# Optimization experiments

Measured on AMD Instinct MI355X. Metric: run time of the kernel, lower is better.

## Reference

```python
import jax, jax.numpy as jnp
import numpy as np

EMBED_DIM = 1024
HIDDEN = 128
N_QUERY = 65536
N_PROTO = 512


def setup_inputs() -> dict:
    key = jax.random.key(0)
    k1, k2, k3, k4, k5, k6, k7 = jax.random.split(key, 7)
    d2 = EMBED_DIM * 2
    lim1 = 1.0 / np.sqrt(d2)
    lim2 = 1.0 / np.sqrt(HIDDEN)
    return {
        "query_features": jax.random.normal(k1, (N_QUERY, EMBED_DIM), dtype=jnp.float32),
        "prototypes": jax.random.normal(k2, (N_PROTO, EMBED_DIM), dtype=jnp.float32),
        "distances": jax.random.uniform(k3, (N_QUERY, N_PROTO), dtype=jnp.float32),
        "W1": jax.random.uniform(k4, (d2, HIDDEN), minval=-lim1, maxval=lim1, dtype=jnp.float32),
        "b1": jax.random.uniform(k5, (HIDDEN,), minval=-lim1, maxval=lim1, dtype=jnp.float32),
        "W2": jax.random.uniform(k6, (HIDDEN, 1), minval=-lim2, maxval=lim2, dtype=jnp.float32),
        "b2": jax.random.uniform(k7, (1,), minval=-lim2, maxval=lim2, dtype=jnp.float32),
    }


def reference(query_features, prototypes, distances, W1, b1, W2, b2):
    # Batched version of the per-query loop: argmin -> gather -> concat -> MLP.
    idx = jnp.argmin(distances, axis=1)                      # [N_QUERY]
    closest = prototypes[idx]                                # [N_QUERY, D]
    combined = jnp.concatenate([query_features, closest], axis=-1)  # [N_QUERY, 2D]
    h = jax.nn.relu(combined @ W1 + b1)                      # [N_QUERY, 128]
    out = jax.nn.sigmoid(h @ W2 + b2)                        # [N_QUERY, 1]
    return jnp.squeeze(out, axis=-1)                         # [N_QUERY]
```

## Files before the change

### kernel.cpp

```cpp
#include <hip/hip_runtime.h>
#include <hip/hip_bf16.h>
#include <math.h>

#define EMBED 1024
#define HIDDEN 128
#define NPROTO 512

typedef short bf16x8 __attribute__((ext_vector_type(8)));
typedef short bf16x4 __attribute__((ext_vector_type(4)));
typedef float f32x4 __attribute__((ext_vector_type(4)));

__device__ __forceinline__ unsigned short f2bf(float x) {
    unsigned u = __builtin_bit_cast(unsigned, x);
    unsigned r = u + 0x7FFFu + ((u >> 16) & 1u);
    return (unsigned short)(r >> 16);
}

__global__ __launch_bounds__(128) void prep_kernel(
    const float* __restrict__ prototypes,
    const float* __restrict__ W1,
    float* __restrict__ proto_h,
    unsigned short* __restrict__ w1t)
{
    int blk = blockIdx.x;
    int t = threadIdx.x;
    if (blk < 64) {
        __shared__ float pl[8][1024];
        int p0 = blk * 8;
        const float4* src = (const float4*)(prototypes + (size_t)p0 * EMBED);
        float4* dst = (float4*)(&pl[0][0]);
        #pragma unroll
        for (int i = 0; i < 16; ++i) dst[t + i * 128] = src[t + i * 128];
        __syncthreads();
        float acc[8] = {0.f,0.f,0.f,0.f,0.f,0.f,0.f,0.f};
        for (int k = 0; k < 1024; k += 8) {
            float w[8];
            #pragma unroll
            for (int j = 0; j < 8; ++j) w[j] = W1[(size_t)(1024 + k + j) * 128 + t];
            #pragma unroll
            for (int j = 0; j < 8; ++j) {
                #pragma unroll
                for (int p = 0; p < 8; ++p) acc[p] += pl[p][k + j] * w[j];
            }
        }
        #pragma unroll
        for (int p = 0; p < 8; ++p) proto_h[(size_t)(p0 + p) * 128 + t] = acc[p];
    } else {
        int b = blk - 64;
        #pragma unroll
        for (int i = 0; i < 16; ++i) {
            int flat = b * 2048 + i * 128 + t;
            int k = flat >> 7;
            int n = flat & 127;
            w1t[(size_t)n * 1024 + k] = f2bf(W1[(size_t)k * 128 + n]);
        }
    }
}

__global__ __launch_bounds__(256) void main_kernel(
    const float* __restrict__ qf,
    const float* __restrict__ dist,
    const float* __restrict__ b1,
    const float* __restrict__ W2,
    const float* __restrict__ b2,
    const float* __restrict__ proto_h,
    const unsigned short* __restrict__ w1t,
    float* __restrict__ out)
{
    const int LDA = 72;
    __shared__ unsigned short a_lds[128 * 72];
    __shared__ unsigned short b_lds[128 * 72];
    __shared__ int s_idx[128];
    __shared__ float s_red[128][2];

    int t = threadIdx.x;
    int wave = t >> 6, lane = t & 63;
    int blk = blockIdx.x;
    int q0 = blk * 128;

    for (int i = 0; i < 32; ++i) {
        int q = wave * 32 + i;
        const float* dr = dist + (size_t)(q0 + q) * 512;
        float4 v0 = ((const float4*)dr)[lane];
        float4 v1 = ((const float4*)dr)[lane + 64];
        float bv = v0.x; int bi = lane * 4;
        if (v0.y < bv) { bv = v0.y; bi = lane * 4 + 1; }
        if (v0.z < bv) { bv = v0.z; bi = lane * 4 + 2; }
        if (v0.w < bv) { bv = v0.w; bi = lane * 4 + 3; }
        int b1i = 256 + lane * 4;
        if (v1.x < bv) { bv = v1.x; bi = b1i; }
        if (v1.y < bv) { bv = v1.y; bi = b1i + 1; }
        if (v1.z < bv) { bv = v1.z; bi = b1i + 2; }
        if (v1.w < bv) { bv = v1.w; bi = b1i + 3; }
        #pragma unroll
        for (int s = 1; s < 64; s <<= 1) {
            float ov = __shfl_xor(bv, s);
            int   oi = __shfl_xor(bi, s);
            if (ov < bv || (ov == bv && oi < bi)) { bv = ov; bi = oi; }
        }
        if (lane == 0) s_idx[q] = bi;
    }

    int wave_m = wave >> 1, wave_n = wave & 1;
    int quad = lane >> 4, tid16 = lane & 15;
    f32x4 acc[4][4];
    #pragma unroll
    for (int mi = 0; mi < 4; ++mi)
        #pragma unroll
        for (int ni = 0; ni < 4; ++ni)
            acc[mi][ni] = (f32x4){0.f, 0.f, 0.f, 0.f};

    for (int kt = 0; kt < 1024; kt += 64) {
        #pragma unroll
        for (int i = 0; i < 8; ++i) {
            int m = (t >> 4) + i * 16;
            int k = (t & 15) * 4;
            float4 v = *(const float4*)(qf + (size_t)(q0 + m) * 1024 + kt + k);
            bf16x4 pk;
            pk.x = (short)f2bf(v.x); pk.y = (short)f2bf(v.y);
            pk.z = (short)f2bf(v.z); pk.w = (short)f2bf(v.w);
            *(bf16x4*)(&a_lds[m * LDA + k]) = pk;
        }
        #pragma unroll
        for (int i = 0; i < 4; ++i) {
            int n = (t >> 3) + i * 32;
            int k = (t & 7) * 8;
            bf16x8 v = *(const bf16x8*)(w1t + (size_t)n * 1024 + kt + k);
            *(bf16x8*)(&b_lds[n * LDA + k]) = v;
        }
        __syncthreads();

        #pragma unroll
        for (int ks = 0; ks < 2; ++ks) {
            int kk = ks * 32 + quad * 8;
            bf16x8 af[4], bfr[4];
            #pragma unroll
            for (int mi = 0; mi < 4; ++mi)
                af[mi] = *(bf16x8*)(&a_lds[(wave_m * 64 + mi * 16 + tid16) * LDA + kk]);
            #pragma unroll
            for (int ni = 0; ni < 4; ++ni)
                bfr[ni] = *(bf16x8*)(&b_lds[(wave_n * 64 + ni * 16 + tid16) * LDA + kk]);
            #pragma unroll
            for (int mi = 0; mi < 4; ++mi)
                #pragma unroll
                for (int ni = 0; ni < 4; ++ni)
                    acc[mi][ni] = __builtin_amdgcn_mfma_f32_16x16x32_bf16(
                        af[mi], bfr[ni], acc[mi][ni], 0, 0, 0);
        }
        __syncthreads();
    }

    float b1v[4], w2v[4];
    #pragma unroll
    for (int ni = 0; ni < 4; ++ni) {
        int n = wave_n * 64 + ni * 16 + tid16;
        b1v[ni] = b1[n];
        w2v[ni] = W2[n];
    }
    #pragma unroll
    for (int mi = 0; mi < 4; ++mi) {
        #pragma unroll
        for (int r = 0; r < 4; ++r) {
            int m = wave_m * 64 + mi * 16 + quad * 4 + r;
            const float* ph = proto_h + (size_t)s_idx[m] * 128;
            float sum = 0.f;
            #pragma unroll
            for (int ni = 0; ni < 4; ++ni) {
                int n = wave_n * 64 + ni * 16 + tid16;
                float v = acc[mi][ni][r] + b1v[ni] + ph[n];
                sum += fmaxf(v, 0.f) * w2v[ni];
            }
            #pragma unroll
            for (int s = 1; s < 16; s <<= 1) sum += __shfl_xor(sum, s);
            if (tid16 == 0) s_red[m][wave_n] = sum;
        }
    }
    __syncthreads();
    if (t < 128) {
        float s = s_red[t][0] + s_red[t][1] + b2[0];
        out[q0 + t] = 1.f / (1.f + expf(-s));
    }
}

extern "C" void kernel_launch(void* const* d_in, const int* in_sizes, int n_in,
                              void* d_out, int out_size, void* d_ws, size_t ws_size,
                              hipStream_t stream) {
    const float* qf    = (const float*)d_in[0];
    const float* proto = (const float*)d_in[1];
    const float* dist  = (const float*)d_in[2];
    const float* W1    = (const float*)d_in[3];
    const float* b1    = (const float*)d_in[4];
    const float* W2    = (const float*)d_in[5];
    const float* b2    = (const float*)d_in[6];
    float* out = (float*)d_out;

    float* proto_h = (float*)d_ws;
    unsigned short* w1t = (unsigned short*)((char*)d_ws + 512 * 128 * 4);

    prep_kernel<<<128, 128, 0, stream>>>(proto, W1, proto_h, w1t);

    int nq = in_sizes[0] / EMBED;
    main_kernel<<<nq / 128, 256, 0, stream>>>(qf, dist, b1, W2, b2, proto_h, w1t, out);
}
```

Measured before the change: 525.3 us.

## Double-buffer query tiles in LDS, load W1 fragments directly, batch argmin loads

The main kernel now double-buffers the bf16 query tile in LDS, prefetching the next K-slice of fp32 query features into registers while the MFMAs on the current slice run. There is one barrier per iteration instead of two. The B operand (transposed bf16 W1) is read straight from global/L2 into registers, so the B LDS tile goes away. The argmin over distances issues four rows' loads at once to raise memory-level parallelism, and the first query tile load is issued before the argmin. The prep kernel is also reorganized with more blocks and vectorized bf16x8 stores. Launch bounds now request 3 blocks per CU, which risks register pressure from the prefetch buffers.

```diff
diff --git a/kernel.cpp b/kernel.cpp
--- a/kernel.cpp
+++ b/kernel.cpp
@@ -5,9 +5,9 @@
 #define EMBED 1024
 #define HIDDEN 128
 #define NPROTO 512
+#define LDA 72
 
 typedef short bf16x8 __attribute__((ext_vector_type(8)));
-typedef short bf16x4 __attribute__((ext_vector_type(4)));
 typedef float f32x4 __attribute__((ext_vector_type(4)));
 
 __device__ __forceinline__ unsigned short f2bf(float x) {
@@ -16,48 +16,39 @@
     return (unsigned short)(r >> 16);
 }
 
-__global__ __launch_bounds__(128) void prep_kernel(
+__global__ __launch_bounds__(256) void prep_kernel(
     const float* __restrict__ prototypes,
     const float* __restrict__ W1,
     float* __restrict__ proto_h,
     unsigned short* __restrict__ w1t)
 {
-    int blk = blockIdx.x;
+    int b = blockIdx.x;
     int t = threadIdx.x;
-    if (blk < 64) {
-        __shared__ float pl[8][1024];
-        int p0 = blk * 8;
-        const float4* src = (const float4*)(prototypes + (size_t)p0 * EMBED);
-        float4* dst = (float4*)(&pl[0][0]);
-        #pragma unroll
-        for (int i = 0; i < 16; ++i) dst[t + i * 128] = src[t + i * 128];
-        __syncthreads();
-        float acc[8] = {0.f,0.f,0.f,0.f,0.f,0.f,0.f,0.f};
-        for (int k = 0; k < 1024; k += 8) {
-            float w[8];
-            #pragma unroll
-            for (int j = 0; j < 8; ++j) w[j] = W1[(size_t)(1024 + k + j) * 128 + t];
-            #pragma unroll
-            for (int j = 0; j < 8; ++j) {
-                #pragma unroll
-                for (int p = 0; p < 8; ++p) acc[p] += pl[p][k + j] * w[j];
-            }
-        }
-        #pragma unroll
-        for (int p = 0; p < 8; ++p) proto_h[(size_t)(p0 + p) * 128 + t] = acc[p];
+    if (b < 256) {
+        int ph = t >> 7, h = t & 127;
+        int p = b * 2 + ph;
+        const float* pr = prototypes + (size_t)p * EMBED;
+        const float* w  = W1 + (size_t)EMBED * HIDDEN + h;
+        float acc = 0.f;
+        for (int k = 0; k < EMBED; k += 8) {
+            #pragma unroll
+            for (int j = 0; j < 8; ++j)
+                acc += pr[k + j] * w[(size_t)(k + j) * HIDDEN];
+        }
+        proto_h[(size_t)p * HIDDEN + h] = acc;
     } else {
-        int b = blk - 64;
-        #pragma unroll
-        for (int i = 0; i < 16; ++i) {
-            int flat = b * 2048 + i * 128 + t;
-            int k = flat >> 7;
-            int n = flat & 127;
-            w1t[(size_t)n * 1024 + k] = f2bf(W1[(size_t)k * 128 + n]);
-        }
-    }
-}
-
-__global__ __launch_bounds__(256) void main_kernel(
+        int s = (b - 256) * 256 + t;
+        int n = s & 127;
+        int k0 = (s >> 7) * 8;
+        bf16x8 v;
+        #pragma unroll
+        for (int j = 0; j < 8; ++j)
+            v[j] = (short)f2bf(W1[(size_t)(k0 + j) * HIDDEN + n]);
+        *(bf16x8*)(w1t + (size_t)n * EMBED + k0) = v;
+    }
+}
+
+__global__ __launch_bounds__(256, 3) void main_kernel(
     const float* __restrict__ qf,
     const float* __restrict__ dist,
     const float* __restrict__ b1,
@@ -67,39 +58,67 @@
     const unsigned short* __restrict__ w1t,
     float* __restrict__ out)
 {
-    const int LDA = 72;
-    __shared__ unsigned short a_lds[128 * 72];
-    __shared__ unsigned short b_lds[128 * 72];
+    __shared__ unsigned short a_lds[2][128 * LDA];
     __shared__ int s_idx[128];
     __shared__ float s_red[128][2];
 
     int t = threadIdx.x;
     int wave = t >> 6, lane = t & 63;
-    int blk = blockIdx.x;
-    int q0 = blk * 128;
-
-    for (int i = 0; i < 32; ++i) {
-        int q = wave * 32 + i;
-        const float* dr = dist + (size_t)(q0 + q) * 512;
-        float4 v0 = ((const float4*)dr)[lane];
-        float4 v1 = ((const float4*)dr)[lane + 64];
-        float bv = v0.x; int bi = lane * 4;
-        if (v0.y < bv) { bv = v0.y; bi = lane * 4 + 1; }
-        if (v0.z < bv) { bv = v0.z; bi = lane * 4 + 2; }
-        if (v0.w < bv) { bv = v0.w; bi = lane * 4 + 3; }
-        int b1i = 256 + lane * 4;
-        if (v1.x < bv) { bv = v1.x; bi = b1i; }
-        if (v1.y < bv) { bv = v1.y; bi = b1i + 1; }
-        if (v1.z < bv) { bv = v1.z; bi = b1i + 2; }
-        if (v1.w < bv) { bv = v1.w; bi = b1i + 3; }
-        #pragma unroll
-        for (int s = 1; s < 64; s <<= 1) {
-            float ov = __shfl_xor(bv, s);
-            int   oi = __shfl_xor(bi, s);
-            if (ov < bv || (ov == bv && oi < bi)) { bv = ov; bi = oi; }
-        }
-        if (lane == 0) s_idx[q] = bi;
-    }
+    int q0 = blockIdx.x * 128;
+
+    int sm = t >> 3;
+    int sk = (t & 7) * 8;
+
+    float4 pre[4][2];
+    {
+        const float* base = qf + (size_t)q0 * EMBED;
+        #pragma unroll
+        for (int i = 0; i < 4; ++i) {
+            const float* src = base + (size_t)(sm + i * 32) * EMBED + sk;
+            pre[i][0] = *(const float4*)src;
+            pre[i][1] = *(const float4*)(src + 4);
+        }
+    }
+
+    for (int i = 0; i < 32; i += 4) {
+        float4 v0[4], v1[4];
+        #pragma unroll
+        for (int j = 0; j < 4; ++j) {
+            const float* dr = dist + (size_t)(q0 + wave * 32 + i + j) * NPROTO;
+            v0[j] = ((const float4*)dr)[lane];
+            v1[j] = ((const float4*)dr)[lane + 64];
+        }
+        #pragma unroll
+        for (int j = 0; j < 4; ++j) {
+            float bv = v0[j].x; int bi = lane * 4;
+            if (v0[j].y < bv) { bv = v0[j].y; bi = lane * 4 + 1; }
+            if (v0[j].z < bv) { bv = v0[j].z; bi = lane * 4 + 2; }
+            if (v0[j].w < bv) { bv = v0[j].w; bi = lane * 4 + 3; }
+            int c = 256 + lane * 4;
+            if (v1[j].x < bv) { bv = v1[j].x; bi = c; }
+            if (v1[j].y < bv) { bv = v1[j].y; bi = c + 1; }
+            if (v1[j].z < bv) { bv = v1[j].z; bi = c + 2; }
+            if (v1[j].w < bv) { bv = v1[j].w; bi = c + 3; }
+            #pragma unroll
+            for (int s = 1; s < 64; s <<= 1) {
+                float ov = __shfl_xor(bv, s);
+                int   oi = __shfl_xor(bi, s);
+                if (ov < bv || (ov == bv && oi < bi)) { bv = ov; bi = oi; }
+            }
+            if (lane == 0) s_idx[wave * 32 + i + j] = bi;
+        }
+    }
+
+    #pragma unroll
+    for (int i = 0; i < 4; ++i) {
+        bf16x8 pk;
+        pk[0] = (short)f2bf(pre[i][0].x); pk[1] = (short)f2bf(pre[i][0].y);
+        pk[2] = (short)f2bf(pre[i][0].z); pk[3] = (short)f2bf(pre[i][0].w);
+        pk[4] = (short)f2bf(pre[i][1].x); pk[5] = (short)f2bf(pre[i][1].y);
+        pk[6] = (short)f2bf(pre[i][1].z); pk[7] = (short)f2bf(pre[i][1].w);
+        *(bf16x8*)(&a_lds[0][(sm + i * 32) * LDA + sk]) = pk;
+    }
+    __syncthreads();
 
     int wave_m = wave >> 1, wave_n = wave & 1;
     int quad = lane >> 4, tid16 = lane & 15;
@@ -110,42 +129,54 @@
         for (int ni = 0; ni < 4; ++ni)
             acc[mi][ni] = (f32x4){0.f, 0.f, 0.f, 0.f};
 
-    for (int kt = 0; kt < 1024; kt += 64) {
-        #pragma unroll
-        for (int i = 0; i < 8; ++i) {
-            int m = (t >> 4) + i * 16;
-            int k = (t & 15) * 4;
-            float4 v = *(const float4*)(qf + (size_t)(q0 + m) * 1024 + kt + k);
-            bf16x4 pk;
-            pk.x = (short)f2bf(v.x); pk.y = (short)f2bf(v.y);
-            pk.z = (short)f2bf(v.z); pk.w = (short)f2bf(v.w);
-            *(bf16x4*)(&a_lds[m * LDA + k]) = pk;
-        }
-        #pragma unroll
-        for (int i = 0; i < 4; ++i) {
-            int n = (t >> 3) + i * 32;
-            int k = (t & 7) * 8;
-            bf16x8 v = *(const bf16x8*)(w1t + (size_t)n * 1024 + kt + k);
-            *(bf16x8*)(&b_lds[n * LDA + k]) = v;
-        }
-        __syncthreads();
+    for (int kt = 0; kt < EMBED; kt += 64) {
+        int cur = (kt >> 6) & 1;
+        bool more = (kt + 64) < EMBED;
+
+        bf16x8 bfr[2][4];
+        #pragma unroll
+        for (int ks = 0; ks < 2; ++ks)
+            #pragma unroll
+            for (int ni = 0; ni < 4; ++ni)
+                bfr[ks][ni] = *(const bf16x8*)(
+                    w1t + (size_t)(wave_n * 64 + ni * 16 + tid16) * EMBED
+                        + kt + ks * 32 + quad * 8);
+
+        if (more) {
+            const float* base = qf + (size_t)q0 * EMBED + kt + 64;
+            #pragma unroll
+            for (int i = 0; i < 4; ++i) {
+                const float* src = base + (size_t)(sm + i * 32) * EMBED + sk;
+                pre[i][0] = *(const float4*)src;
+                pre[i][1] = *(const float4*)(src + 4);
+            }
+        }
 
         #pragma unroll
         for (int ks = 0; ks < 2; ++ks) {
             int kk = ks * 32 + quad * 8;
-            bf16x8 af[4], bfr[4];
+            bf16x8 af[4];
             #pragma unroll
             for (int mi = 0; mi < 4; ++mi)
-                af[mi] = *(bf16x8*)(&a_lds[(wave_m * 64 + mi * 16 + tid16) * LDA + kk]);
-            #pragma unroll
-            for (int ni = 0; ni < 4; ++ni)
-                bfr[ni] = *(bf16x8*)(&b_lds[(wave_n * 64 + ni * 16 + tid16) * LDA + kk]);
+                af[mi] = *(bf16x8*)(&a_lds[cur][(wave_m * 64 + mi * 16 + tid16) * LDA + kk]);
             #pragma unroll
             for (int mi = 0; mi < 4; ++mi)
                 #pragma unroll
                 for (int ni = 0; ni < 4; ++ni)
                     acc[mi][ni] = __builtin_amdgcn_mfma_f32_16x16x32_bf16(
-                        af[mi], bfr[ni], acc[mi][ni], 0, 0, 0);
+                        af[mi], bfr[ks][ni], acc[mi][ni], 0, 0, 0);
+        }
+
+        if (more) {
+            #pragma unroll
+            for (int i = 0; i < 4; ++i) {
+                bf16x8 pk;
+                pk[0] = (short)f2bf(pre[i][0].x); pk[1] = (short)f2bf(pre[i][0].y);
+                pk[2] = (short)f2bf(pre[i][0].z); pk[3] = (short)f2bf(pre[i][0].w);
+                pk[4] = (short)f2bf(pre[i][1].x); pk[5] = (short)f2bf(pre[i][1].y);
+                pk[6] = (short)f2bf(pre[i][1].z); pk[7] = (short)f2bf(pre[i][1].w);
+                *(bf16x8*)(&a_lds[cur ^ 1][(sm + i * 32) * LDA + sk]) = pk;
+            }
         }
         __syncthreads();
     }
@@ -162,7 +193,7 @@
         #pragma unroll
         for (int r = 0; r < 4; ++r) {
             int m = wave_m * 64 + mi * 16 + quad * 4 + r;
-            const float* ph = proto_h + (size_t)s_idx[m] * 128;
+            const float* ph = proto_h + (size_t)s_idx[m] * HIDDEN;
             float sum = 0.f;
             #pragma unroll
             for (int ni = 0; ni < 4; ++ni) {
@@ -197,7 +228,7 @@
     float* proto_h = (float*)d_ws;
     unsigned short* w1t = (unsigned short*)((char*)d_ws + 512 * 128 * 4);
 
-    prep_kernel<<<128, 128, 0, stream>>>(proto, W1, proto_h, w1t);
+    prep_kernel<<<320, 256, 0, stream>>>(proto, W1, proto_h, w1t);
 
     int nq = in_sizes[0] / EMBED;
     main_kernel<<<nq / 128, 256, 0, stream>>>(qf, dist, b1, W2, b2, proto_h, w1t, out);
```

Result: faster. 504.1 us (-4.0%).
